# Kernel optimization log

Hardware: AMD Instinct MI355X
Metric: run time of the kernel (lower is better)

The kernel has to match this reference:

```python
import jax, jax.numpy as jnp
import numpy as np

K = 3  # knnLoss default k


def _knn_loss(source_pc, target_pc, k=K):
    """Faithful translation of knnLoss.forward.

    For each batch: drop exact-zero (0,0,0) points from both clouds
    (emulated via masking for static shapes), find the k nearest *target*
    points for every *source* point (query=source, ref=target), take the
    mean Euclidean distance, then average over batch.
    """

    def per_batch(src, tgt):  # src, tgt: [N, 3]
        src_valid = jnp.any(src != 0.0, axis=-1)  # [Ns] move_zero_point mask
        tgt_valid = jnp.any(tgt != 0.0, axis=-1)  # [Nt]
        s2 = jnp.sum(src * src, axis=-1)          # [Ns]
        t2 = jnp.sum(tgt * tgt, axis=-1)          # [Nt]
        # squared pairwise distances, [Ns, Nt]
        d2 = s2[:, None] + t2[None, :] - 2.0 * (src @ tgt.T)
        d2 = jnp.maximum(d2, 0.0)
        # invalid (zero) target points can never be a neighbor
        d2 = jnp.where(tgt_valid[None, :], d2, jnp.inf)
        neg_top, _ = jax.lax.top_k(-d2, k)        # k smallest squared dists
        dist = jnp.sqrt(-neg_top)                 # [Ns, k] euclidean, like KNN_CUDA
        # mean over valid source points x k neighbors
        num = jnp.sum(jnp.where(src_valid[:, None], dist, 0.0))
        den = jnp.sum(src_valid).astype(dist.dtype) * k
        return num / den

    return jnp.mean(jax.vmap(per_batch)(source_pc, target_pc))


def setup_inputs() -> dict:
    key = jax.random.key(0)
    k1, k2 = jax.random.split(key)
    B, N = 4, 8192
    source_pc = jax.random.normal(k1, (B, N, 3), dtype=jnp.float32)
    target_pc = jax.random.normal(k2, (B, N, 3), dtype=jnp.float32)
    return {"source_pc": source_pc, "target_pc": target_pc}


def reference(source_pc, target_pc):
    return _knn_loss(source_pc, target_pc)
```

## Files before the change

### kernel.cpp

```cpp
#include <hip/hip_runtime.h>
#include <math.h>

#define BATCH 4
#define NPTS 8192
#define TILE 512
#define TSPLIT 16
#define SRC_PER_BLOCK 512
#define SRC_CHUNKS 16
#define NSRC_TOT (BATCH * NPTS)

typedef __attribute__((ext_vector_type(2))) float f2;

__device__ __forceinline__ void insert3(float d, float& a0, float& a1, float& a2) {
    float h = fmaxf(a1, d);
    float m = __builtin_amdgcn_fmed3f(a0, a1, d);
    a2 = fminf(a2, h);
    a1 = m;
    a0 = fminf(a0, d);
}

__device__ __forceinline__ void merge33(float a0, float a1, float a2,
                                        float& b0, float& b1, float& b2) {
    float s0 = fminf(a0, b0);
    float h  = fmaxf(a0, b0);
    float m  = fminf(a1, b1);
    float mm = fminf(a2, b2);
    b1 = fminf(h, m);
    b2 = __builtin_amdgcn_fmed3f(h, m, mm);
    b0 = s0;
}

__global__ __launch_bounds__(256) void knn_partial(const float* __restrict__ src,
                                                   const float* __restrict__ tgt,
                                                   float* __restrict__ part,
                                                   float* __restrict__ hdr) {
    __shared__ float4 ts[TILE / 2 * 2];
    const int tid = threadIdx.x;
    const int sc = blockIdx.x, tc = blockIdx.y, b = blockIdx.z;

    if (sc == 0 && tc == 0 && b == 0 && tid < 16) hdr[tid] = 0.0f;

    {
        const float* tb = tgt + ((size_t)b * NPTS + (size_t)tc * TILE + 2 * tid) * 3;
        float x0 = tb[0], y0 = tb[1], z0 = tb[2];
        float x1 = tb[3], y1 = tb[4], z1 = tb[5];
        float w0 = x0 * x0 + y0 * y0 + z0 * z0;
        float w1 = x1 * x1 + y1 * y1 + z1 * z1;
        if (!(x0 != 0.f || y0 != 0.f || z0 != 0.f)) w0 = 3.0e38f;
        if (!(x1 != 0.f || y1 != 0.f || z1 != 0.f)) w1 = 3.0e38f;
        ts[2 * tid + 0] = make_float4(x0, x1, y0, y1);
        ts[2 * tid + 1] = make_float4(z0, z1, w0, w1);
    }
    __syncthreads();

    f2 nx[2], ny[2], nz[2], s2[2];
    #pragma unroll
    for (int s = 0; s < 2; ++s) {
        int i = sc * SRC_PER_BLOCK + tid + 256 * s;
        const float* sp = src + ((size_t)b * NPTS + i) * 3;
        float ax = sp[0], ay = sp[1], az = sp[2];
        float q = ax * ax + ay * ay + az * az;
        nx[s] = (f2){-2.f * ax, -2.f * ax};
        ny[s] = (f2){-2.f * ay, -2.f * ay};
        nz[s] = (f2){-2.f * az, -2.f * az};
        s2[s] = (f2){q, q};
    }

    float c0[2][2], c1[2][2], c2[2][2];
    #pragma unroll
    for (int s = 0; s < 2; ++s)
        for (int h = 0; h < 2; ++h) { c0[s][h] = c1[s][h] = c2[s][h] = 3e38f; }

    #pragma unroll 4
    for (int e = 0; e < TILE / 2; ++e) {
        float4 p = ts[2 * e + 0];
        float4 q = ts[2 * e + 1];
        f2 xs = (f2){p.x, p.y};
        f2 ys = (f2){p.z, p.w};
        f2 zs = (f2){q.x, q.y};
        f2 ws = (f2){q.z, q.w};
        #pragma unroll
        for (int s = 0; s < 2; ++s) {
            f2 acc = ws + s2[s];
            acc = __builtin_elementwise_fma(zs, nz[s], acc);
            acc = __builtin_elementwise_fma(ys, ny[s], acc);
            acc = __builtin_elementwise_fma(xs, nx[s], acc);
            insert3(acc.x, c0[s][0], c1[s][0], c2[s][0]);
            insert3(acc.y, c0[s][1], c1[s][1], c2[s][1]);
        }
    }

    #pragma unroll
    for (int s = 0; s < 2; ++s) {
        merge33(c0[s][1], c1[s][1], c2[s][1], c0[s][0], c1[s][0], c2[s][0]);
        size_t flat = (size_t)b * NPTS + sc * SRC_PER_BLOCK + tid + 256 * s;
        part[((size_t)tc * 3 + 0) * NSRC_TOT + flat] = c0[s][0];
        part[((size_t)tc * 3 + 1) * NSRC_TOT + flat] = c1[s][0];
        part[((size_t)tc * 3 + 2) * NSRC_TOT + flat] = c2[s][0];
    }
}

__global__ __launch_bounds__(256) void knn_merge(const float* __restrict__ src,
                                                 const float* __restrict__ part,
                                                 float* __restrict__ acc,
                                                 float* __restrict__ cnt,
                                                 unsigned* __restrict__ ticket,
                                                 float* __restrict__ out) {
    const int gid = blockIdx.x * 256 + threadIdx.x;
    const int b = gid >> 13;

    float t0[4], t1[4], t2[4];
    #pragma unroll
    for (int c = 0; c < 4; ++c) { t0[c] = t1[c] = t2[c] = 3e38f; }
    #pragma unroll
    for (int q = 0; q < TSPLIT * 3; ++q)
        insert3(part[(size_t)q * NSRC_TOT + gid], t0[q & 3], t1[q & 3], t2[q & 3]);
    merge33(t0[1], t1[1], t2[1], t0[0], t1[0], t2[0]);
    merge33(t0[3], t1[3], t2[3], t0[2], t1[2], t2[2]);
    merge33(t0[2], t1[2], t2[2], t0[0], t1[0], t2[0]);

    float sx = src[(size_t)gid * 3 + 0];
    float sy = src[(size_t)gid * 3 + 1];
    float sz = src[(size_t)gid * 3 + 2];
    bool valid = (sx != 0.f) || (sy != 0.f) || (sz != 0.f);
    float s = valid ? (sqrtf(fmaxf(t0[0], 0.f)) + sqrtf(fmaxf(t1[0], 0.f)) +
                       sqrtf(fmaxf(t2[0], 0.f)))
                    : 0.f;
    float c = valid ? 1.f : 0.f;

    for (int off = 32; off >= 1; off >>= 1) {
        s += __shfl_down(s, off);
        c += __shfl_down(c, off);
    }
    __shared__ float red_s[4], red_c[4];
    int wave = threadIdx.x >> 6, lane = threadIdx.x & 63;
    if (lane == 0) { red_s[wave] = s; red_c[wave] = c; }
    __syncthreads();
    if (threadIdx.x == 0) {
        atomicAdd(&acc[b], red_s[0] + red_s[1] + red_s[2] + red_s[3]);
        atomicAdd(&cnt[b], red_c[0] + red_c[1] + red_c[2] + red_c[3]);
        __threadfence();
        unsigned t = atomicAdd(ticket, 1u);
        if (t == (unsigned)(gridDim.x - 1)) {
            float loss = 0.f;
            #pragma unroll
            for (int bb = 0; bb < BATCH; ++bb) {
                float as = atomicAdd(&acc[bb], 0.f);
                float ac = atomicAdd(&cnt[bb], 0.f);
                loss += as / (ac * 3.0f);
            }
            out[0] = loss * (1.0f / BATCH);
        }
    }
}

extern "C" void kernel_launch(void* const* d_in, const int* in_sizes, int n_in,
                              void* d_out, int out_size, void* d_ws, size_t ws_size,
                              hipStream_t stream) {
    const float* src = (const float*)d_in[0];
    const float* tgt = (const float*)d_in[1];
    float* out = (float*)d_out;

    float* hdr = (float*)d_ws;
    float* acc = hdr;
    float* cnt = hdr + 4;
    unsigned* ticket = (unsigned*)((char*)d_ws + 32);
    float* part = (float*)((char*)d_ws + 256);

    dim3 g1(SRC_CHUNKS, TSPLIT, BATCH);
    knn_partial<<<g1, 256, 0, stream>>>(src, tgt, part, hdr);

    knn_merge<<<dim3(NSRC_TOT / 256), 256, 0, stream>>>(src, part, acc, cnt, ticket, out);
}
```

Measured before the change: 117.3 us.

## Drop per-source norm from inner loop and use inline packed FMA

Rewrites the distance as 0.5*|t|^2 - s·t so the source norm is a per-row constant added back in the merge kernel, which removes one packed add per pair in the hot loop. The packed FMAs are now emitted as explicit v_pk_fma_f32 inline asm, the unroll factor goes from 4 to 8, and the merge kernel uses 128-thread blocks. The ranking is unchanged because the dropped term is constant per source row. The risks are rounding differences from the reformulated distance and inline asm limiting compiler scheduling.

```diff
diff --git a/kernel.cpp b/kernel.cpp
--- a/kernel.cpp
+++ b/kernel.cpp
@@ -10,6 +10,13 @@
 #define NSRC_TOT (BATCH * NPTS)
 
 typedef __attribute__((ext_vector_type(2))) float f2;
+typedef __attribute__((ext_vector_type(4))) float f4;
+
+__device__ __forceinline__ f2 pk_fma(f2 a, f2 b, f2 c) {
+    f2 d;
+    asm("v_pk_fma_f32 %0, %1, %2, %3" : "=v"(d) : "v"(a), "v"(b), "v"(c));
+    return d;
+}
 
 __device__ __forceinline__ void insert3(float d, float& a0, float& a1, float& a2) {
     float h = fmaxf(a1, d);
@@ -34,7 +41,7 @@
                                                    const float* __restrict__ tgt,
                                                    float* __restrict__ part,
                                                    float* __restrict__ hdr) {
-    __shared__ float4 ts[TILE / 2 * 2];
+    __shared__ f4 ts[TILE / 2 * 2];
     const int tid = threadIdx.x;
     const int sc = blockIdx.x, tc = blockIdx.y, b = blockIdx.z;
 
@@ -44,26 +51,24 @@
         const float* tb = tgt + ((size_t)b * NPTS + (size_t)tc * TILE + 2 * tid) * 3;
         float x0 = tb[0], y0 = tb[1], z0 = tb[2];
         float x1 = tb[3], y1 = tb[4], z1 = tb[5];
-        float w0 = x0 * x0 + y0 * y0 + z0 * z0;
-        float w1 = x1 * x1 + y1 * y1 + z1 * z1;
-        if (!(x0 != 0.f || y0 != 0.f || z0 != 0.f)) w0 = 3.0e38f;
-        if (!(x1 != 0.f || y1 != 0.f || z1 != 0.f)) w1 = 3.0e38f;
-        ts[2 * tid + 0] = make_float4(x0, x1, y0, y1);
-        ts[2 * tid + 1] = make_float4(z0, z1, w0, w1);
+        float w0 = 0.5f * (x0 * x0 + y0 * y0 + z0 * z0);
+        float w1 = 0.5f * (x1 * x1 + y1 * y1 + z1 * z1);
+        if (!(x0 != 0.f || y0 != 0.f || z0 != 0.f)) w0 = 1.0e38f;
+        if (!(x1 != 0.f || y1 != 0.f || z1 != 0.f)) w1 = 1.0e38f;
+        ts[2 * tid + 0] = (f4){x0, x1, y0, y1};
+        ts[2 * tid + 1] = (f4){z0, z1, w0, w1};
     }
     __syncthreads();
 
-    f2 nx[2], ny[2], nz[2], s2[2];
+    f2 nx[2], ny[2], nz[2];
     #pragma unroll
     for (int s = 0; s < 2; ++s) {
         int i = sc * SRC_PER_BLOCK + tid + 256 * s;
         const float* sp = src + ((size_t)b * NPTS + i) * 3;
         float ax = sp[0], ay = sp[1], az = sp[2];
-        float q = ax * ax + ay * ay + az * az;
-        nx[s] = (f2){-2.f * ax, -2.f * ax};
-        ny[s] = (f2){-2.f * ay, -2.f * ay};
-        nz[s] = (f2){-2.f * az, -2.f * az};
-        s2[s] = (f2){q, q};
+        nx[s] = (f2){-ax, -ax};
+        ny[s] = (f2){-ay, -ay};
+        nz[s] = (f2){-az, -az};
     }
 
     float c0[2][2], c1[2][2], c2[2][2];
@@ -71,22 +76,21 @@
     for (int s = 0; s < 2; ++s)
         for (int h = 0; h < 2; ++h) { c0[s][h] = c1[s][h] = c2[s][h] = 3e38f; }
 
-    #pragma unroll 4
+    #pragma unroll 8
     for (int e = 0; e < TILE / 2; ++e) {
-        float4 p = ts[2 * e + 0];
-        float4 q = ts[2 * e + 1];
-        f2 xs = (f2){p.x, p.y};
-        f2 ys = (f2){p.z, p.w};
-        f2 zs = (f2){q.x, q.y};
-        f2 ws = (f2){q.z, q.w};
+        f4 p = ts[2 * e + 0];
+        f4 q = ts[2 * e + 1];
+        f2 xs = __builtin_shufflevector(p, p, 0, 1);
+        f2 ys = __builtin_shufflevector(p, p, 2, 3);
+        f2 zs = __builtin_shufflevector(q, q, 0, 1);
+        f2 wh = __builtin_shufflevector(q, q, 2, 3);
         #pragma unroll
         for (int s = 0; s < 2; ++s) {
-            f2 acc = ws + s2[s];
-            acc = __builtin_elementwise_fma(zs, nz[s], acc);
-            acc = __builtin_elementwise_fma(ys, ny[s], acc);
-            acc = __builtin_elementwise_fma(xs, nx[s], acc);
-            insert3(acc.x, c0[s][0], c1[s][0], c2[s][0]);
-            insert3(acc.y, c0[s][1], c1[s][1], c2[s][1]);
+            f2 v = pk_fma(xs, nx[s], wh);
+            v = pk_fma(ys, ny[s], v);
+            v = pk_fma(zs, nz[s], v);
+            insert3(v.x, c0[s][0], c1[s][0], c2[s][0]);
+            insert3(v.y, c0[s][1], c1[s][1], c2[s][1]);
         }
     }
 
@@ -100,13 +104,13 @@
     }
 }
 
-__global__ __launch_bounds__(256) void knn_merge(const float* __restrict__ src,
+__global__ __launch_bounds__(128) void knn_merge(const float* __restrict__ src,
                                                  const float* __restrict__ part,
                                                  float* __restrict__ acc,
                                                  float* __restrict__ cnt,
                                                  unsigned* __restrict__ ticket,
                                                  float* __restrict__ out) {
-    const int gid = blockIdx.x * 256 + threadIdx.x;
+    const int gid = blockIdx.x * 128 + threadIdx.x;
     const int b = gid >> 13;
 
     float t0[4], t1[4], t2[4];
@@ -122,23 +126,25 @@
     float sx = src[(size_t)gid * 3 + 0];
     float sy = src[(size_t)gid * 3 + 1];
     float sz = src[(size_t)gid * 3 + 2];
+    float s2 = sx * sx + sy * sy + sz * sz;
     bool valid = (sx != 0.f) || (sy != 0.f) || (sz != 0.f);
-    float s = valid ? (sqrtf(fmaxf(t0[0], 0.f)) + sqrtf(fmaxf(t1[0], 0.f)) +
-                       sqrtf(fmaxf(t2[0], 0.f)))
-                    : 0.f;
+    float d0 = sqrtf(fmaxf(fmaf(2.f, t0[0], s2), 0.f));
+    float d1 = sqrtf(fmaxf(fmaf(2.f, t1[0], s2), 0.f));
+    float d2 = sqrtf(fmaxf(fmaf(2.f, t2[0], s2), 0.f));
+    float s = valid ? (d0 + d1 + d2) : 0.f;
     float c = valid ? 1.f : 0.f;
 
     for (int off = 32; off >= 1; off >>= 1) {
         s += __shfl_down(s, off);
         c += __shfl_down(c, off);
     }
-    __shared__ float red_s[4], red_c[4];
+    __shared__ float red_s[2], red_c[2];
     int wave = threadIdx.x >> 6, lane = threadIdx.x & 63;
     if (lane == 0) { red_s[wave] = s; red_c[wave] = c; }
     __syncthreads();
     if (threadIdx.x == 0) {
-        atomicAdd(&acc[b], red_s[0] + red_s[1] + red_s[2] + red_s[3]);
-        atomicAdd(&cnt[b], red_c[0] + red_c[1] + red_c[2] + red_c[3]);
+        atomicAdd(&acc[b], red_s[0] + red_s[1]);
+        atomicAdd(&cnt[b], red_c[0] + red_c[1]);
         __threadfence();
         unsigned t = atomicAdd(ticket, 1u);
         if (t == (unsigned)(gridDim.x - 1)) {
@@ -170,5 +176,5 @@
     dim3 g1(SRC_CHUNKS, TSPLIT, BATCH);
     knn_partial<<<g1, 256, 0, stream>>>(src, tgt, part, hdr);
 
-    knn_merge<<<dim3(NSRC_TOT / 256), 256, 0, stream>>>(src, part, acc, cnt, ticket, out);
+    knn_merge<<<dim3(NSRC_TOT / 128), 128, 0, stream>>>(src, part, acc, cnt, ticket, out);
 }
```

After: 123.0 us. +4.9%, slower.

## Compute pairwise distances with bf16 split-precision MFMA instead of FP32 FMAs

Applied to the files above, without the earlier changes.

Replaces the scalar FP32 distance loop with 16x16x32 bf16 MFMA, where each coordinate and squared norm is split into hi/lo bf16 parts so the products approximate FP32 precision. Target points are pre-packed into MFMA B-fragments by a small prep kernel. Each wave now scans the whole target set for 16 sources and reduces top-3 across lanes with shuffles, which removes the partial-result buffer and merge pass. The catch is a longer serial loop per wave with only 512 blocks, and approximation error from the bf16 split, notably the missing xl*yl-style cross terms.

```diff
diff --git a/kernel.cpp b/kernel.cpp
--- a/kernel.cpp
+++ b/kernel.cpp
@@ -3,13 +3,18 @@
 
 #define BATCH 4
 #define NPTS 8192
-#define TILE 512
-#define TSPLIT 16
-#define SRC_PER_BLOCK 512
-#define SRC_CHUNKS 16
-#define NSRC_TOT (BATCH * NPTS)
+#define TILES 512
 
-typedef __attribute__((ext_vector_type(2))) float f2;
+typedef __attribute__((ext_vector_type(8))) short short8;
+typedef __attribute__((ext_vector_type(4))) float floatx4;
+
+__device__ __forceinline__ unsigned short bf16hi(float v) {
+    unsigned u = __float_as_uint(v);
+    return (unsigned short)((u + 0x7FFFu + ((u >> 16) & 1u)) >> 16);
+}
+__device__ __forceinline__ float bf16f(unsigned short h) {
+    return __uint_as_float(((unsigned)h) << 16);
+}
 
 __device__ __forceinline__ void insert3(float d, float& a0, float& a1, float& a2) {
     float h = fmaxf(a1, d);
@@ -30,123 +35,125 @@
     b0 = s0;
 }
 
-__global__ __launch_bounds__(256) void knn_partial(const float* __restrict__ src,
-                                                   const float* __restrict__ tgt,
-                                                   float* __restrict__ part,
-                                                   float* __restrict__ hdr) {
-    __shared__ float4 ts[TILE / 2 * 2];
+__global__ __launch_bounds__(256) void knn_prep(const float* __restrict__ tgt,
+                                                short8* __restrict__ packed,
+                                                float* __restrict__ hdr) {
+    int gid = blockIdx.x * 256 + threadIdx.x;
+    if (gid < 16) hdr[gid] = 0.0f;
+    int lane = gid & 31;
+    int bt = gid >> 5;
+    int n = lane & 15;
+    int q = lane >> 4;
+    int batch = bt >> 9, tile = bt & 511;
+    const float* tp = tgt + ((size_t)batch * NPTS + tile * 16 + n) * 3;
+    float x = tp[0], y = tp[1], z = tp[2];
+    float t2 = x * x + y * y + z * z;
+    if (!(x != 0.f || y != 0.f || z != 0.f)) t2 = 3.0e38f;
+    unsigned short xh = bf16hi(x),  xl = bf16hi(x - bf16f(xh));
+    unsigned short yh = bf16hi(y),  yl = bf16hi(y - bf16f(yh));
+    unsigned short zh = bf16hi(z),  zl = bf16hi(z - bf16f(zh));
+    unsigned short th = bf16hi(t2), tl = bf16hi(t2 - bf16f(th));
+    const short one = (short)0x3F80;
+    short8 v;
+    if (q == 0)
+        v = (short8){(short)xh, (short)xl, (short)xh, (short)yh,
+                     (short)yl, (short)yh, (short)zh, (short)zl};
+    else
+        v = (short8){(short)zh, one, one, (short)th, (short)tl, 0, 0, 0};
+    packed[(size_t)bt * 32 + lane] = v;
+}
+
+__global__ __launch_bounds__(256) void knn_main(const float* __restrict__ src,
+                                                const short8* __restrict__ packed,
+                                                float* __restrict__ acc,
+                                                float* __restrict__ cnt,
+                                                unsigned* __restrict__ ticket,
+                                                float* __restrict__ out) {
     const int tid = threadIdx.x;
-    const int sc = blockIdx.x, tc = blockIdx.y, b = blockIdx.z;
+    const int wave = tid >> 6, lane = tid & 63;
+    const int b = blockIdx.z;
+    const int sg = blockIdx.x * 4 + wave;
+    const int m = lane & 15, q = lane >> 4;
 
-    if (sc == 0 && tc == 0 && b == 0 && tid < 16) hdr[tid] = 0.0f;
+    const float* sp = src + ((size_t)b * NPTS + sg * 16 + m) * 3;
+    float sx = sp[0], sy = sp[1], sz = sp[2];
+    float s2 = sx * sx + sy * sy + sz * sz;
+    float mx = -2.f * sx, my = -2.f * sy, mz = -2.f * sz;
+    unsigned short xh = bf16hi(mx), xl = bf16hi(mx - bf16f(xh));
+    unsigned short yh = bf16hi(my), yl = bf16hi(my - bf16f(yh));
+    unsigned short zh = bf16hi(mz), zl = bf16hi(mz - bf16f(zh));
+    unsigned short sh = bf16hi(s2), sl = bf16hi(s2 - bf16f(sh));
+    const short one = (short)0x3F80;
+    short8 afrag = (short8){0, 0, 0, 0, 0, 0, 0, 0};
+    if (q == 0)
+        afrag = (short8){(short)xh, (short)xh, (short)xl, (short)yh,
+                         (short)yh, (short)yl, (short)zh, (short)zh};
+    else if (q == 1)
+        afrag = (short8){(short)zl, (short)sh, (short)sl, one, one, 0, 0, 0};
 
-    {
-        const float* tb = tgt + ((size_t)b * NPTS + (size_t)tc * TILE + 2 * tid) * 3;
-        float x0 = tb[0], y0 = tb[1], z0 = tb[2];
-        float x1 = tb[3], y1 = tb[4], z1 = tb[5];
-        float w0 = x0 * x0 + y0 * y0 + z0 * z0;
-        float w1 = x1 * x1 + y1 * y1 + z1 * z1;
-        if (!(x0 != 0.f || y0 != 0.f || z0 != 0.f)) w0 = 3.0e38f;
-        if (!(x1 != 0.f || y1 != 0.f || z1 != 0.f)) w1 = 3.0e38f;
-        ts[2 * tid + 0] = make_float4(x0, x1, y0, y1);
-        ts[2 * tid + 1] = make_float4(z0, z1, w0, w1);
-    }
-    __syncthreads();
+    float t0[4], t1[4], t2[4];
+    #pragma unroll
+    for (int j = 0; j < 4; ++j) { t0[j] = t1[j] = t2[j] = 3e38f; }
 
-    f2 nx[2], ny[2], nz[2], s2[2];
-    #pragma unroll
-    for (int s = 0; s < 2; ++s) {
-        int i = sc * SRC_PER_BLOCK + tid + 256 * s;
-        const float* sp = src + ((size_t)b * NPTS + i) * 3;
-        float ax = sp[0], ay = sp[1], az = sp[2];
-        float q = ax * ax + ay * ay + az * az;
-        nx[s] = (f2){-2.f * ax, -2.f * ax};
-        ny[s] = (f2){-2.f * ay, -2.f * ay};
-        nz[s] = (f2){-2.f * az, -2.f * az};
-        s2[s] = (f2){q, q};
+    const short8* bb = packed + (size_t)b * TILES * 32 + (lane & 31);
+
+    #pragma unroll 4
+    for (int tile = 0; tile < TILES; ++tile) {
+        short8 bfrag = bb[(size_t)tile * 32];
+        floatx4 c = {0.f, 0.f, 0.f, 0.f};
+        c = __builtin_amdgcn_mfma_f32_16x16x32_bf16(afrag, bfrag, c, 0, 0, 0);
+        insert3(c[0], t0[0], t1[0], t2[0]);
+        insert3(c[1], t0[1], t1[1], t2[1]);
+        insert3(c[2], t0[2], t1[2], t2[2]);
+        insert3(c[3], t0[3], t1[3], t2[3]);
     }
 
-    float c0[2][2], c1[2][2], c2[2][2];
     #pragma unroll
-    for (int s = 0; s < 2; ++s)
-        for (int h = 0; h < 2; ++h) { c0[s][h] = c1[s][h] = c2[s][h] = 3e38f; }
-
-    #pragma unroll 4
-    for (int e = 0; e < TILE / 2; ++e) {
-        float4 p = ts[2 * e + 0];
-        float4 q = ts[2 * e + 1];
-        f2 xs = (f2){p.x, p.y};
-        f2 ys = (f2){p.z, p.w};
-        f2 zs = (f2){q.x, q.y};
-        f2 ws = (f2){q.z, q.w};
+    for (int mask = 1; mask <= 8; mask <<= 1) {
         #pragma unroll
-        for (int s = 0; s < 2; ++s) {
-            f2 acc = ws + s2[s];
-            acc = __builtin_elementwise_fma(zs, nz[s], acc);
-            acc = __builtin_elementwise_fma(ys, ny[s], acc);
-            acc = __builtin_elementwise_fma(xs, nx[s], acc);
-            insert3(acc.x, c0[s][0], c1[s][0], c2[s][0]);
-            insert3(acc.y, c0[s][1], c1[s][1], c2[s][1]);
+        for (int j = 0; j < 4; ++j) {
+            float b0 = __shfl_xor(t0[j], mask);
+            float b1 = __shfl_xor(t1[j], mask);
+            float b2 = __shfl_xor(t2[j], mask);
+            merge33(b0, b1, b2, t0[j], t1[j], t2[j]);
         }
     }
 
-    #pragma unroll
-    for (int s = 0; s < 2; ++s) {
-        merge33(c0[s][1], c1[s][1], c2[s][1], c0[s][0], c1[s][0], c2[s][0]);
-        size_t flat = (size_t)b * NPTS + sc * SRC_PER_BLOCK + tid + 256 * s;
-        part[((size_t)tc * 3 + 0) * NSRC_TOT + flat] = c0[s][0];
-        part[((size_t)tc * 3 + 1) * NSRC_TOT + flat] = c1[s][0];
-        part[((size_t)tc * 3 + 2) * NSRC_TOT + flat] = c2[s][0];
+    int cc = lane & 15;
+    float dsum = 0.f, dcnt = 0.f;
+    if (cc < 4) {
+        float m0 = t0[0], m1 = t1[0], m2 = t2[0];
+        if (cc == 1) { m0 = t0[1]; m1 = t1[1]; m2 = t2[1]; }
+        if (cc == 2) { m0 = t0[2]; m1 = t1[2]; m2 = t2[2]; }
+        if (cc == 3) { m0 = t0[3]; m1 = t1[3]; m2 = t2[3]; }
+        int row = q * 4 + cc;
+        const float* vp = src + ((size_t)b * NPTS + sg * 16 + row) * 3;
+        float vx = vp[0], vy = vp[1], vz = vp[2];
+        if (vx != 0.f || vy != 0.f || vz != 0.f) {
+            dsum = sqrtf(fmaxf(m0, 0.f)) + sqrtf(fmaxf(m1, 0.f)) +
+                   sqrtf(fmaxf(m2, 0.f));
+            dcnt = 1.f;
+        }
     }
-}
-
-__global__ __launch_bounds__(256) void knn_merge(const float* __restrict__ src,
-                                                 const float* __restrict__ part,
-                                                 float* __restrict__ acc,
-                                                 float* __restrict__ cnt,
-                                                 unsigned* __restrict__ ticket,
-                                                 float* __restrict__ out) {
-    const int gid = blockIdx.x * 256 + threadIdx.x;
-    const int b = gid >> 13;
-
-    float t0[4], t1[4], t2[4];
-    #pragma unroll
-    for (int c = 0; c < 4; ++c) { t0[c] = t1[c] = t2[c] = 3e38f; }
-    #pragma unroll
-    for (int q = 0; q < TSPLIT * 3; ++q)
-        insert3(part[(size_t)q * NSRC_TOT + gid], t0[q & 3], t1[q & 3], t2[q & 3]);
-    merge33(t0[1], t1[1], t2[1], t0[0], t1[0], t2[0]);
-    merge33(t0[3], t1[3], t2[3], t0[2], t1[2], t2[2]);
-    merge33(t0[2], t1[2], t2[2], t0[0], t1[0], t2[0]);
-
-    float sx = src[(size_t)gid * 3 + 0];
-    float sy = src[(size_t)gid * 3 + 1];
-    float sz = src[(size_t)gid * 3 + 2];
-    bool valid = (sx != 0.f) || (sy != 0.f) || (sz != 0.f);
-    float s = valid ? (sqrtf(fmaxf(t0[0], 0.f)) + sqrtf(fmaxf(t1[0], 0.f)) +
-                       sqrtf(fmaxf(t2[0], 0.f)))
-                    : 0.f;
-    float c = valid ? 1.f : 0.f;
-
     for (int off = 32; off >= 1; off >>= 1) {
-        s += __shfl_down(s, off);
-        c += __shfl_down(c, off);
+        dsum += __shfl_down(dsum, off);
+        dcnt += __shfl_down(dcnt, off);
     }
-    __shared__ float red_s[4], red_c[4];
-    int wave = threadIdx.x >> 6, lane = threadIdx.x & 63;
-    if (lane == 0) { red_s[wave] = s; red_c[wave] = c; }
+    __shared__ float rs[4], rc[4];
+    if (lane == 0) { rs[wave] = dsum; rc[wave] = dcnt; }
     __syncthreads();
-    if (threadIdx.x == 0) {
-        atomicAdd(&acc[b], red_s[0] + red_s[1] + red_s[2] + red_s[3]);
-        atomicAdd(&cnt[b], red_c[0] + red_c[1] + red_c[2] + red_c[3]);
+    if (tid == 0) {
+        atomicAdd(&acc[b], rs[0] + rs[1] + rs[2] + rs[3]);
+        atomicAdd(&cnt[b], rc[0] + rc[1] + rc[2] + rc[3]);
         __threadfence();
         unsigned t = atomicAdd(ticket, 1u);
-        if (t == (unsigned)(gridDim.x - 1)) {
+        unsigned total = gridDim.x * gridDim.y * gridDim.z;
+        if (t == total - 1) {
             float loss = 0.f;
             #pragma unroll
-            for (int bb = 0; bb < BATCH; ++bb) {
-                float as = atomicAdd(&acc[bb], 0.f);
-                float ac = atomicAdd(&cnt[bb], 0.f);
+            for (int bb2 = 0; bb2 < BATCH; ++bb2) {
+                float as = atomicAdd(&acc[bb2], 0.f);
+                float ac = atomicAdd(&cnt[bb2], 0.f);
                 loss += as / (ac * 3.0f);
             }
             out[0] = loss * (1.0f / BATCH);
@@ -165,10 +172,10 @@
     float* acc = hdr;
     float* cnt = hdr + 4;
     unsigned* ticket = (unsigned*)((char*)d_ws + 32);
-    float* part = (float*)((char*)d_ws + 256);
+    short8* packed = (short8*)((char*)d_ws + 4096);
 
-    dim3 g1(SRC_CHUNKS, TSPLIT, BATCH);
-    knn_partial<<<g1, 256, 0, stream>>>(src, tgt, part, hdr);
+    knn_prep<<<dim3(256), 256, 0, stream>>>(tgt, packed, hdr);
 
-    knn_merge<<<dim3(NSRC_TOT / 256), 256, 0, stream>>>(src, part, acc, cnt, ticket, out);
+    knn_main<<<dim3(128, 1, BATCH), 256, 0, stream>>>(src, packed, acc, cnt,
+                                                      ticket, out);
 }
```

After: 166.9 us. 42.2% more time.
